# Kernel tuning notes

Hardware: AMD Instinct MI355X
Metric: run time of the kernel (lower is better)

Reference implementation:

```python
import jax, jax.numpy as jnp
import numpy as np

B, M, H = 8, 2048, 1024


def setup_inputs() -> dict:
    key = jax.random.key(0)
    k0, k1, k2, k3, k4 = jax.random.split(key, 5)
    return {
        "query": jax.random.normal(k0, (B, M, H), dtype=jnp.float32),
        "key": jax.random.normal(k1, (B, M, H), dtype=jnp.float32),
        "span": jax.random.uniform(k2, (B, M, 2), dtype=jnp.float32),
        "value": jax.random.normal(k3, (B, M, H), dtype=jnp.float32),
        "key_pe": jax.random.normal(k4, (1, H, M), dtype=jnp.float32),
    }


def reference(query, key, span, value, key_pe):
    # Faithful to the source's returned value:
    #   attn_cont (span-gathered version) is overwritten by the dense q @ k^T,
    #   and the scaled/softmaxed `attn` (content + positional) is computed but
    #   NEVER used for the output. The module returns attn_cont @ value with
    #   no scaling and no softmax. span / key_pe do not affect the output.
    attn_cont = jnp.einsum('bmh,bnh->bmn', query, key)  # [B, M, M]
    out = jnp.matmul(attn_cont, value)                   # [B, M, H]
    return out
```

## Files before the change

### kernel.cpp

```cpp
#include <hip/hip_runtime.h>
#include <hip/hip_bf16.h>

typedef __attribute__((ext_vector_type(4))) float f32x4;
typedef __attribute__((ext_vector_type(8))) short bf16x8;
typedef unsigned short u16;


__device__ __forceinline__ u16 f2bf(float f) {
  union { float f; unsigned int u; } v;
  v.f = f;
  unsigned int r = (v.u + 0x7fffu + ((v.u >> 16) & 1u)) >> 16;
  return (u16)r;
}

__device__ __forceinline__ void async16(const void* g, const void* l) {
  __builtin_amdgcn_global_load_lds(
      (const __attribute__((address_space(1))) unsigned int*)(unsigned long)g,
      (__attribute__((address_space(3))) unsigned int*)(unsigned int)(unsigned long)l,
      16, 0, 0);
}


__global__ __launch_bounds__(256) void cvt_plain(const float* __restrict__ in,
                                                 u16* __restrict__ out, int n4) {
  int stride = gridDim.x * blockDim.x;
  for (int i = blockIdx.x * blockDim.x + threadIdx.x; i < n4; i += stride) {
    f32x4 v = *(const f32x4*)(in + (long)i * 4);
    ushort4 o;
    o.x = f2bf(v.x); o.y = f2bf(v.y); o.z = f2bf(v.z); o.w = f2bf(v.w);
    *(ushort4*)(out + (long)i * 4) = o;
  }
}


__global__ __launch_bounds__(256) void cvt_transpose(const float* __restrict__ in,
                                                     u16* __restrict__ out,
                                                     int R, int C) {
  __shared__ u16 tile[64][68];
  const long bo = (long)blockIdx.z * (long)R * (long)C;
  const int r0 = blockIdx.y * 64;
  const int c0 = blockIdx.x * 64;
  const int t = threadIdx.x;
  const int tr = t >> 4;
  const int tc4 = (t & 15) * 4;

#pragma unroll
  for (int i = 0; i < 4; ++i) {
    int r = i * 16 + tr;
    f32x4 v = *(const f32x4*)(in + bo + (long)(r0 + r) * C + c0 + tc4);
    tile[tc4 + 0][r] = f2bf(v.x);
    tile[tc4 + 1][r] = f2bf(v.y);
    tile[tc4 + 2][r] = f2bf(v.z);
    tile[tc4 + 3][r] = f2bf(v.w);
  }
  __syncthreads();
#pragma unroll
  for (int i = 0; i < 4; ++i) {
    int c = i * 16 + tr;
    ushort4 u = *(const ushort4*)(&tile[c][tc4]);
    *(ushort4*)(out + bo + (long)(c0 + c) * R + r0 + tc4) = u;
  }
}


#define BM 128
#define BN 128
#define BK 32

template <bool BF16OUT>
__global__ __launch_bounds__(256, 4) void gemm_nt(const u16* __restrict__ A,
                                                  const u16* __restrict__ Bt,
                                                  void* __restrict__ Cv,
                                                  int M, int N, int K,
                                                  long sA, long sB, long sC,
                                                  int nTN) {
  __shared__ u16 As[2][BM][BK];
  __shared__ u16 Bs[2][BN][BK];

  const int bid  = blockIdx.x;
  const int b    = bid & 7;
  const int tile = bid >> 3;
  const int bn0 = (tile % nTN) * BN;
  const int bm0 = (tile / nTN) * BM;

  A  += (long)b * sA;
  Bt += (long)b * sB;

  const int tid  = threadIdx.x;
  const int lane = tid & 63;
  const int wave = tid >> 6;
  const int wr = wave >> 1;
  const int wc = wave & 1;
  const int l16 = lane & 15;
  const int kh  = lane >> 4;

  const u16* Abase = A + (long)bm0 * K;
  const u16* Bbase = Bt + (long)bn0 * K;

  const int u0 = wave * 64 + lane;

  f32x4 acc[4][4] = {};

  const int NT = K / BK;
  int cur = 0;

#pragma unroll
  for (int i = 0; i < 2; ++i) {
    int u = i * 256 + u0;
    async16(Abase + (long)(u >> 2) * K + (u & 3) * 8,
            (const char*)(&As[0][0][0]) + i * 4096 + wave * 1024);
    async16(Bbase + (long)(u >> 2) * K + (u & 3) * 8,
            (const char*)(&Bs[0][0][0]) + i * 4096 + wave * 1024);
  }
  asm volatile("s_waitcnt vmcnt(0)" ::: "memory");
  __syncthreads();

  for (int t = 0; t < NT; ++t) {
    if (t + 1 < NT) {
      const int k0 = (t + 1) * BK;
      const int nb = cur ^ 1;
#pragma unroll
      for (int i = 0; i < 2; ++i) {
        int u = i * 256 + u0;
        async16(Abase + k0 + (long)(u >> 2) * K + (u & 3) * 8,
                (const char*)(&As[nb][0][0]) + i * 4096 + wave * 1024);
        async16(Bbase + k0 + (long)(u >> 2) * K + (u & 3) * 8,
                (const char*)(&Bs[nb][0][0]) + i * 4096 + wave * 1024);
      }
    }

    bf16x8 af[4], bfr[4];
#pragma unroll
    for (int i = 0; i < 4; ++i) {
      af[i]  = *(const bf16x8*)(&As[cur][wr * 64 + i * 16 + l16][kh * 8]);
      bfr[i] = *(const bf16x8*)(&Bs[cur][wc * 64 + i * 16 + l16][kh * 8]);
    }
#pragma unroll
    for (int i = 0; i < 4; ++i)
#pragma unroll
      for (int j = 0; j < 4; ++j)
        acc[i][j] =
            __builtin_amdgcn_mfma_f32_16x16x32_bf16(af[i], bfr[j], acc[i][j], 0, 0, 0);

    asm volatile("s_waitcnt vmcnt(0)" ::: "memory");
    __syncthreads();
    cur ^= 1;
  }

  u16*   Cb = (u16*)Cv + (long)b * sC;
  float* Cf = (float*)Cv + (long)b * sC;
#pragma unroll
  for (int i = 0; i < 4; ++i) {
    const int gm = bm0 + wr * 64 + i * 16 + kh * 4;
#pragma unroll
    for (int j = 0; j < 4; ++j) {
      const int gn = bn0 + wc * 64 + j * 16 + l16;
#pragma unroll
      for (int r = 0; r < 4; ++r) {
        if (BF16OUT)
          Cb[(long)(gm + r) * N + gn] = f2bf(acc[i][j][r]);
        else
          Cf[(long)(gm + r) * N + gn] = acc[i][j][r];
      }
    }
  }
}


extern "C" void kernel_launch(void* const* d_in, const int* in_sizes, int n_in,
                              void* d_out, int out_size, void* d_ws, size_t ws_size,
                              hipStream_t stream) {
  const float* Q  = (const float*)d_in[0];
  const float* Kf = (const float*)d_in[1];
  const float* V  = (const float*)d_in[3];
  float* out = (float*)d_out;

  const int B = 8, M = 2048, H = 1024;
  const size_t bmh2 = (size_t)B * M * H * 2;

  char* ws = (char*)d_ws;
  u16* Qb = (u16*)(ws);
  u16* Kt = (u16*)(ws + bmh2);
  u16* Vt = (u16*)(ws + 2 * bmh2);
  u16* Pt = (u16*)(ws + 3 * bmh2);

  cvt_plain<<<2048, 256, 0, stream>>>(Q, Qb, B * M * H / 4);
  cvt_transpose<<<dim3(H / 64, M / 64, B), 256, 0, stream>>>(Kf, Kt, M, H);
  cvt_transpose<<<dim3(H / 64, M / 64, B), 256, 0, stream>>>(V, Vt, M, H);

  gemm_nt<true><<<B * (H / BM) * (H / BN), 256, 0, stream>>>(
      Vt, Kt, (void*)Pt, H, H, M, (long)H * M, (long)H * M, (long)H * H, H / BN);

  gemm_nt<false><<<B * (M / BM) * (H / BN), 256, 0, stream>>>(
      Qb, Pt, (void*)out, M, H, H, (long)M * H, (long)H * H, (long)M * H, H / BN);
}
```

Baseline: 151.7 us.

## Rewrite GEMM with 256x128 tiles, 8 waves, triple-buffered swizzled LDS pipeline

Replaces the 128x128x32 double-buffered GEMM with a 512-thread kernel using 256x128 tiles, BK=64, three LDS stages, and an XOR swizzle on LDS rows to avoid bank conflicts. Global-to-LDS async loads are interleaved between MFMA groups, with barriers and setprio so memory traffic overlaps compute. The aim is better data reuse per block, fewer bank conflicts and hidden load latency. In exchange it uses more LDS and registers per block and launches fewer blocks, which lowers occupancy.

```diff
diff --git a/kernel.cpp b/kernel.cpp
--- a/kernel.cpp
+++ b/kernel.cpp
@@ -63,104 +63,161 @@
 }
 
 
-#define BM 128
-#define BN 128
-#define BK 32
+#define ASTRIDE (256 * 64)
+#define BSTRIDE (128 * 64)
+
+#define LD_A(c, f, ks) (*(const bf16x8*)((const u16*)As + (c)*ASTRIDE + offA[f][ks]))
+#define LD_B(c, f, ks) (*(const bf16x8*)((const u16*)Bs + (c)*BSTRIDE + offB[f][ks]))
+#define STG_A(i, buf) async16(srcA[i], (const char*)As + (buf)*(ASTRIDE * 2) + dstA[i])
+#define STG_B(i, buf) async16(srcB[i], (const char*)Bs + (buf)*(BSTRIDE * 2) + dstB[i])
+#define MF(am, bn, fm, fn) \
+  acc[fm][fn] = __builtin_amdgcn_mfma_f32_16x16x32_bf16(am, bn, acc[fm][fn], 0, 0, 0)
 
 template <bool BF16OUT>
-__global__ __launch_bounds__(256, 4) void gemm_nt(const u16* __restrict__ A,
-                                                  const u16* __restrict__ Bt,
-                                                  void* __restrict__ Cv,
-                                                  int M, int N, int K,
-                                                  long sA, long sB, long sC,
-                                                  int nTN) {
-  __shared__ u16 As[2][BM][BK];
-  __shared__ u16 Bs[2][BN][BK];
+__global__ __launch_bounds__(512, 2) void gemm8(const u16* __restrict__ A,
+                                                const u16* __restrict__ Bt,
+                                                void* __restrict__ Cv,
+                                                int M, int N, int K,
+                                                long sA, long sB, long sC,
+                                                int nTN) {
+  __shared__ u16 As[3][256][64];
+  __shared__ u16 Bs[3][128][64];
 
   const int bid  = blockIdx.x;
   const int b    = bid & 7;
   const int tile = bid >> 3;
-  const int bn0 = (tile % nTN) * BN;
-  const int bm0 = (tile / nTN) * BM;
-
-  A  += (long)b * sA;
-  Bt += (long)b * sB;
+  const int bn0 = (tile % nTN) * 128;
+  const int bm0 = (tile / nTN) * 256;
+
+  const u16* Ab = A + (long)b * sA + (long)bm0 * K;
+  const u16* Bb = Bt + (long)b * sB + (long)bn0 * K;
 
   const int tid  = threadIdx.x;
   const int lane = tid & 63;
   const int wave = tid >> 6;
-  const int wr = wave >> 1;
-  const int wc = wave & 1;
-  const int l16 = lane & 15;
-  const int kh  = lane >> 4;
-
-  const u16* Abase = A + (long)bm0 * K;
-  const u16* Bbase = Bt + (long)bn0 * K;
-
-  const int u0 = wave * 64 + lane;
+  const int wr   = wave >> 1;
+  const int wc   = wave & 1;
+  const int l16  = lane & 15;
+  const int kh   = lane >> 4;
+
+  const char* srcA[4];
+  const char* srcB[2];
+  int dstA[4], dstB[2];
+#pragma unroll
+  for (int i = 0; i < 4; ++i) {
+    int u = tid + i * 512;
+    int row = u >> 3, sl = (u & 7) ^ (row & 7);
+    srcA[i] = (const char*)(Ab + (long)row * K) + sl * 16;
+    dstA[i] = u * 16;
+  }
+#pragma unroll
+  for (int i = 0; i < 2; ++i) {
+    int u = tid + i * 512;
+    int row = u >> 3, sl = (u & 7) ^ (row & 7);
+    srcB[i] = (const char*)(Bb + (long)row * K) + sl * 16;
+    dstB[i] = u * 16;
+  }
+
+  int offA[4][2], offB[4][2];
+#pragma unroll
+  for (int f = 0; f < 4; ++f) {
+    int rA = wr * 64 + f * 16 + l16;
+    int rB = wc * 64 + f * 16 + l16;
+#pragma unroll
+    for (int ks = 0; ks < 2; ++ks) {
+      offA[f][ks] = rA * 64 + (((ks * 4 + kh) ^ (rA & 7)) * 8);
+      offB[f][ks] = rB * 64 + (((ks * 4 + kh) ^ (rB & 7)) * 8);
+    }
+  }
 
   f32x4 acc[4][4] = {};
-
-  const int NT = K / BK;
-  int cur = 0;
-
-#pragma unroll
-  for (int i = 0; i < 2; ++i) {
-    int u = i * 256 + u0;
-    async16(Abase + (long)(u >> 2) * K + (u & 3) * 8,
-            (const char*)(&As[0][0][0]) + i * 4096 + wave * 1024);
-    async16(Bbase + (long)(u >> 2) * K + (u & 3) * 8,
-            (const char*)(&Bs[0][0][0]) + i * 4096 + wave * 1024);
-  }
-  asm volatile("s_waitcnt vmcnt(0)" ::: "memory");
-  __syncthreads();
-
+  const int NT = K / 64;
+
+#pragma unroll
+  for (int i = 0; i < 4; ++i) STG_A(i, 0);
+#pragma unroll
+  for (int i = 0; i < 2; ++i) STG_B(i, 0);
+#pragma unroll
+  for (int i = 0; i < 4; ++i) srcA[i] += 128;
+#pragma unroll
+  for (int i = 0; i < 2; ++i) srcB[i] += 128;
+#pragma unroll
+  for (int i = 0; i < 4; ++i) STG_A(i, 1);
+#pragma unroll
+  for (int i = 0; i < 2; ++i) STG_B(i, 1);
+#pragma unroll
+  for (int i = 0; i < 4; ++i) srcA[i] += 128;
+#pragma unroll
+  for (int i = 0; i < 2; ++i) srcB[i] += 128;
+  asm volatile("s_waitcnt vmcnt(6)" ::: "memory");
+  __builtin_amdgcn_s_barrier();
+
+  int c = 0, nb = 2;
   for (int t = 0; t < NT; ++t) {
-    if (t + 1 < NT) {
-      const int k0 = (t + 1) * BK;
-      const int nb = cur ^ 1;
-#pragma unroll
-      for (int i = 0; i < 2; ++i) {
-        int u = i * 256 + u0;
-        async16(Abase + k0 + (long)(u >> 2) * K + (u & 3) * 8,
-                (const char*)(&As[nb][0][0]) + i * 4096 + wave * 1024);
-        async16(Bbase + k0 + (long)(u >> 2) * K + (u & 3) * 8,
-                (const char*)(&Bs[nb][0][0]) + i * 4096 + wave * 1024);
-      }
-    }
-
-    bf16x8 af[4], bfr[4];
-#pragma unroll
-    for (int i = 0; i < 4; ++i) {
-      af[i]  = *(const bf16x8*)(&As[cur][wr * 64 + i * 16 + l16][kh * 8]);
-      bfr[i] = *(const bf16x8*)(&Bs[cur][wc * 64 + i * 16 + l16][kh * 8]);
-    }
-#pragma unroll
-    for (int i = 0; i < 4; ++i)
-#pragma unroll
-      for (int j = 0; j < 4; ++j)
-        acc[i][j] =
-            __builtin_amdgcn_mfma_f32_16x16x32_bf16(af[i], bfr[j], acc[i][j], 0, 0, 0);
-
-    asm volatile("s_waitcnt vmcnt(0)" ::: "memory");
-    __syncthreads();
-    cur ^= 1;
+    const bool st = (t + 2) < NT;
+
+    bf16x8 a0 = LD_A(c, 0, 0), a1 = LD_A(c, 1, 0);
+    bf16x8 b0 = LD_B(c, 0, 0), b1 = LD_B(c, 1, 0);
+    bf16x8 b2 = LD_B(c, 2, 0), b3 = LD_B(c, 3, 0);
+    if (st) { STG_A(0, nb); STG_A(1, nb); }
+    asm volatile("" ::: "memory");
+    __builtin_amdgcn_s_barrier();
+    __builtin_amdgcn_s_setprio(1);
+    MF(a0, b0, 0, 0); MF(a0, b1, 0, 1); MF(a0, b2, 0, 2); MF(a0, b3, 0, 3);
+    MF(a1, b0, 1, 0); MF(a1, b1, 1, 1); MF(a1, b2, 1, 2); MF(a1, b3, 1, 3);
+    __builtin_amdgcn_s_setprio(0);
+
+    bf16x8 a2 = LD_A(c, 2, 0), a3 = LD_A(c, 3, 0);
+    if (st) { STG_A(2, nb); STG_A(3, nb); }
+    asm volatile("" ::: "memory");
+    __builtin_amdgcn_s_barrier();
+    __builtin_amdgcn_s_setprio(1);
+    MF(a2, b0, 2, 0); MF(a2, b1, 2, 1); MF(a2, b2, 2, 2); MF(a2, b3, 2, 3);
+    MF(a3, b0, 3, 0); MF(a3, b1, 3, 1); MF(a3, b2, 3, 2); MF(a3, b3, 3, 3);
+    __builtin_amdgcn_s_setprio(0);
+
+    a0 = LD_A(c, 0, 1); a1 = LD_A(c, 1, 1);
+    b0 = LD_B(c, 0, 1); b1 = LD_B(c, 1, 1);
+    b2 = LD_B(c, 2, 1); b3 = LD_B(c, 3, 1);
+    if (st) STG_B(0, nb);
+    asm volatile("" ::: "memory");
+    __builtin_amdgcn_s_barrier();
+    __builtin_amdgcn_s_setprio(1);
+    MF(a0, b0, 0, 0); MF(a0, b1, 0, 1); MF(a0, b2, 0, 2); MF(a0, b3, 0, 3);
+    MF(a1, b0, 1, 0); MF(a1, b1, 1, 1); MF(a1, b2, 1, 2); MF(a1, b3, 1, 3);
+    __builtin_amdgcn_s_setprio(0);
+
+    a2 = LD_A(c, 2, 1); a3 = LD_A(c, 3, 1);
+    if (st) STG_B(1, nb);
+#pragma unroll
+    for (int i = 0; i < 4; ++i) srcA[i] += 128;
+#pragma unroll
+    for (int i = 0; i < 2; ++i) srcB[i] += 128;
+    if (st) asm volatile("s_waitcnt vmcnt(6)" ::: "memory");
+    else    asm volatile("s_waitcnt vmcnt(0)" ::: "memory");
+    asm volatile("s_waitcnt lgkmcnt(0)" ::: "memory");
+    __builtin_amdgcn_s_barrier();
+    __builtin_amdgcn_s_setprio(1);
+    MF(a2, b0, 2, 0); MF(a2, b1, 2, 1); MF(a2, b2, 2, 2); MF(a2, b3, 2, 3);
+    MF(a3, b0, 3, 0); MF(a3, b1, 3, 1); MF(a3, b2, 3, 2); MF(a3, b3, 3, 3);
+    __builtin_amdgcn_s_setprio(0);
+
+    c = (c == 2) ? 0 : c + 1;
+    nb = (nb == 2) ? 0 : nb + 1;
   }
 
   u16*   Cb = (u16*)Cv + (long)b * sC;
   float* Cf = (float*)Cv + (long)b * sC;
 #pragma unroll
-  for (int i = 0; i < 4; ++i) {
-    const int gm = bm0 + wr * 64 + i * 16 + kh * 4;
-#pragma unroll
-    for (int j = 0; j < 4; ++j) {
-      const int gn = bn0 + wc * 64 + j * 16 + l16;
+  for (int fm = 0; fm < 4; ++fm) {
+    const int gm = bm0 + wr * 64 + fm * 16 + kh * 4;
+#pragma unroll
+    for (int fn = 0; fn < 4; ++fn) {
+      const int gn = bn0 + wc * 64 + fn * 16 + l16;
 #pragma unroll
       for (int r = 0; r < 4; ++r) {
-        if (BF16OUT)
-          Cb[(long)(gm + r) * N + gn] = f2bf(acc[i][j][r]);
-        else
-          Cf[(long)(gm + r) * N + gn] = acc[i][j][r];
+        if (BF16OUT) Cb[(long)(gm + r) * N + gn] = f2bf(acc[fm][fn][r]);
+        else         Cf[(long)(gm + r) * N + gn] = acc[fm][fn][r];
       }
     }
   }
@@ -188,9 +245,11 @@
   cvt_transpose<<<dim3(H / 64, M / 64, B), 256, 0, stream>>>(Kf, Kt, M, H);
   cvt_transpose<<<dim3(H / 64, M / 64, B), 256, 0, stream>>>(V, Vt, M, H);
 
-  gemm_nt<true><<<B * (H / BM) * (H / BN), 256, 0, stream>>>(
-      Vt, Kt, (void*)Pt, H, H, M, (long)H * M, (long)H * M, (long)H * H, H / BN);
-
-  gemm_nt<false><<<B * (M / BM) * (H / BN), 256, 0, stream>>>(
-      Qb, Pt, (void*)out, M, H, H, (long)M * H, (long)H * H, (long)M * H, H / BN);
-}
+  gemm8<true><<<8 * (1024 / 256) * (1024 / 128), 512, 0, stream>>>(
+      Vt, Kt, (void*)Pt, 1024, 1024, 2048, (long)H * M, (long)H * M, (long)H * H,
+      1024 / 128);
+
+  gemm8<false><<<8 * (2048 / 256) * (1024 / 128), 512, 0, stream>>>(
+      Qb, Pt, (void*)out, 2048, 1024, 1024, (long)M * H, (long)H * H, (long)M * H,
+      1024 / 128);
+}
```

Result: faster. 143.3 us (-5.6%).

## Replace GEMM with 8-wave ping-pong pipelined kernel using larger swizzled tiles

Applied to the files above, without the earlier changes.

Replaces the 4-wave 128x128x32 double-buffered GEMM with an 8-wave kernel that uses larger tiles (128x256 and 256x256) and BK=64. The tiles are split into half-quadrants with XOR-swizzled LDS layout. Global-to-LDS loads are interleaved with MFMA quadrants, using fine-grained barriers, partial vmcnt waits and s_setprio, so memory traffic overlaps compute. This aims to cut LDS bank conflicts and global traffic per FLOP and to hide load latency, at the cost of higher register pressure and more barriers.

```diff
diff --git a/kernel.cpp b/kernel.cpp
--- a/kernel.cpp
+++ b/kernel.cpp
@@ -63,104 +63,175 @@
 }
 
 
-#define BM 128
-#define BN 128
-#define BK 32
-
-template <bool BF16OUT>
-__global__ __launch_bounds__(256, 4) void gemm_nt(const u16* __restrict__ A,
-                                                  const u16* __restrict__ Bt,
-                                                  void* __restrict__ Cv,
-                                                  int M, int N, int K,
-                                                  long sA, long sB, long sC,
-                                                  int nTN) {
-  __shared__ u16 As[2][BM][BK];
-  __shared__ u16 Bs[2][BN][BK];
-
-  const int bid  = blockIdx.x;
-  const int b    = bid & 7;
+#define BARRIER()                                   \
+  {                                                 \
+    asm volatile("" ::: "memory");                  \
+    __builtin_amdgcn_s_barrier();                   \
+    asm volatile("" ::: "memory");                  \
+  }
+
+#define STG_A(h, buf)                                                         \
+  {                                                                           \
+    _Pragma("unroll") for (int i_ = 0; i_ < LA; ++i_) {                       \
+      async16(Ab + aoff[h][i_],                                               \
+              (char*)&As[buf][h][0][0] + (tid + i_ * 512) * 16);              \
+      aoff[h][i_] += 128;                                                     \
+    }                                                                         \
+  }
+
+#define STG_B(h, buf)                                                         \
+  {                                                                           \
+    _Pragma("unroll") for (int i_ = 0; i_ < LB; ++i_) {                       \
+      async16(Bb + boff[h][i_],                                               \
+              (char*)&Bs[buf][h][0][0] + (tid + i_ * 512) * 16);              \
+      boff[h][i_] += 128;                                                     \
+    }                                                                         \
+  }
+
+#define LDA_Q(buf, qm)                                                        \
+  {                                                                           \
+    _Pragma("unroll") for (int f_ = 0; f_ < HM; ++f_) {                       \
+      areg[f_][0] = *(const bf16x8*)&As[buf][qm][wrA + f_ * 16][sw0];         \
+      areg[f_][1] = *(const bf16x8*)&As[buf][qm][wrA + f_ * 16][sw1];         \
+    }                                                                         \
+  }
+
+#define LDB_Q(buf, qn)                                                        \
+  {                                                                           \
+    _Pragma("unroll") for (int g_ = 0; g_ < HN; ++g_) {                       \
+      breg[qn * HN + g_][0] = *(const bf16x8*)&Bs[buf][qn][wcB + g_ * 16][sw0]; \
+      breg[qn * HN + g_][1] = *(const bf16x8*)&Bs[buf][qn][wcB + g_ * 16][sw1]; \
+    }                                                                         \
+  }
+
+#define MMA_Q(qm, qn)                                                         \
+  {                                                                           \
+    __builtin_amdgcn_s_setprio(1);                                            \
+    _Pragma("unroll") for (int f_ = 0; f_ < HM; ++f_)                         \
+    _Pragma("unroll") for (int g_ = 0; g_ < HN; ++g_)                         \
+    _Pragma("unroll") for (int k_ = 0; k_ < 2; ++k_)                          \
+      acc[qm * HM + f_][qn * HN + g_] =                                       \
+          __builtin_amdgcn_mfma_f32_16x16x32_bf16(                            \
+              areg[f_][k_], breg[qn * HN + g_][k_],                           \
+              acc[qm * HM + f_][qn * HN + g_], 0, 0, 0);                      \
+    __builtin_amdgcn_s_setprio(0);                                            \
+  }
+
+#define VMC_LA()                                                              \
+  {                                                                           \
+    if constexpr (LA == 2) asm volatile("s_waitcnt vmcnt(2)" ::: "memory");   \
+    else asm volatile("s_waitcnt vmcnt(1)" ::: "memory");                     \
+  }
+
+#define VMC_STEADY()                                                          \
+  {                                                                           \
+    if (more) VMC_LA()                                                        \
+    else asm volatile("s_waitcnt vmcnt(0)" ::: "memory");                     \
+  }
+
+#define TILE(cur, nxt, g01, g23, vm)                                          \
+  {                                                                           \
+                                          \
+    LDA_Q(cur, 0); LDB_Q(cur, 0);                                             \
+    if (g01) STG_A(1, nxt);                                                   \
+    BARRIER(); MMA_Q(0, 0); BARRIER();                                        \
+                                          \
+    LDB_Q(cur, 1);                                                            \
+    if (g01) STG_B(0, nxt);                                                   \
+    BARRIER(); MMA_Q(0, 1); BARRIER();                                        \
+                                          \
+    LDA_Q(cur, 1);                                                            \
+    if (g01) STG_B(1, nxt);                                                   \
+    BARRIER(); MMA_Q(1, 0); BARRIER();                                        \
+                          \
+    if (g23) STG_A(0, cur);                                                   \
+    vm;                                                                       \
+    BARRIER(); MMA_Q(1, 1); BARRIER();                                        \
+  }
+
+template <int BM, int BN, bool BF16OUT>
+__global__ __launch_bounds__(512, 2) void gemm8p(const u16* __restrict__ A,
+                                                 const u16* __restrict__ Bt,
+                                                 void* __restrict__ Cv,
+                                                 int N, int K,
+                                                 long sA, long sB, long sC,
+                                                 int nTN) {
+  constexpr int FM = BM / 32;
+  constexpr int FN = BN / 64;
+  constexpr int HM = FM / 2, HN = FN / 2;
+  constexpr int LA = BM / 128, LB = BN / 128;
+
+  __shared__ u16 As[2][2][BM / 2][64];
+  __shared__ u16 Bs[2][2][BN / 2][64];
+
+  const int bid = blockIdx.x;
+  const int b = bid & 7;
   const int tile = bid >> 3;
   const int bn0 = (tile % nTN) * BN;
   const int bm0 = (tile / nTN) * BM;
 
-  A  += (long)b * sA;
-  Bt += (long)b * sB;
-
-  const int tid  = threadIdx.x;
+  const char* Ab = (const char*)(A + (long)b * sA);
+  const char* Bb = (const char*)(Bt + (long)b * sB);
+
+  const int tid = threadIdx.x;
   const int lane = tid & 63;
   const int wave = tid >> 6;
-  const int wr = wave >> 1;
-  const int wc = wave & 1;
+  const int wr = wave >> 2;
+  const int wc = wave & 3;
   const int l16 = lane & 15;
-  const int kh  = lane >> 4;
-
-  const u16* Abase = A + (long)bm0 * K;
-  const u16* Bbase = Bt + (long)bn0 * K;
-
-  const int u0 = wave * 64 + lane;
-
-  f32x4 acc[4][4] = {};
-
-  const int NT = K / BK;
-  int cur = 0;
-
-#pragma unroll
-  for (int i = 0; i < 2; ++i) {
-    int u = i * 256 + u0;
-    async16(Abase + (long)(u >> 2) * K + (u & 3) * 8,
-            (const char*)(&As[0][0][0]) + i * 4096 + wave * 1024);
-    async16(Bbase + (long)(u >> 2) * K + (u & 3) * 8,
-            (const char*)(&Bs[0][0][0]) + i * 4096 + wave * 1024);
-  }
-  asm volatile("s_waitcnt vmcnt(0)" ::: "memory");
-  __syncthreads();
-
-  for (int t = 0; t < NT; ++t) {
-    if (t + 1 < NT) {
-      const int k0 = (t + 1) * BK;
-      const int nb = cur ^ 1;
-#pragma unroll
-      for (int i = 0; i < 2; ++i) {
-        int u = i * 256 + u0;
-        async16(Abase + k0 + (long)(u >> 2) * K + (u & 3) * 8,
-                (const char*)(&As[nb][0][0]) + i * 4096 + wave * 1024);
-        async16(Bbase + k0 + (long)(u >> 2) * K + (u & 3) * 8,
-                (const char*)(&Bs[nb][0][0]) + i * 4096 + wave * 1024);
-      }
+  const int kh = lane >> 4;
+
+  const int wrA = wr * (HM * 16) + l16;
+  const int wcB = wc * (HN * 16) + l16;
+  const int sw0 = (kh ^ (l16 & 7)) * 8;
+  const int sw1 = ((4 + kh) ^ (l16 & 7)) * 8;
+
+  int aoff[2][LA], boff[2][LB];
+#pragma unroll
+  for (int h = 0; h < 2; ++h)
+#pragma unroll
+    for (int i = 0; i < LA; ++i) {
+      int u = tid + i * 512;
+      int row = u >> 3, sl = (u & 7) ^ (row & 7);
+      aoff[h][i] = (bm0 + h * (BM / 2) + row) * (K * 2) + sl * 16;
     }
-
-    bf16x8 af[4], bfr[4];
-#pragma unroll
-    for (int i = 0; i < 4; ++i) {
-      af[i]  = *(const bf16x8*)(&As[cur][wr * 64 + i * 16 + l16][kh * 8]);
-      bfr[i] = *(const bf16x8*)(&Bs[cur][wc * 64 + i * 16 + l16][kh * 8]);
+#pragma unroll
+  for (int h = 0; h < 2; ++h)
+#pragma unroll
+    for (int i = 0; i < LB; ++i) {
+      int u = tid + i * 512;
+      int row = u >> 3, sl = (u & 7) ^ (row & 7);
+      boff[h][i] = (bn0 + h * (BN / 2) + row) * (K * 2) + sl * 16;
     }
-#pragma unroll
-    for (int i = 0; i < 4; ++i)
-#pragma unroll
-      for (int j = 0; j < 4; ++j)
-        acc[i][j] =
-            __builtin_amdgcn_mfma_f32_16x16x32_bf16(af[i], bfr[j], acc[i][j], 0, 0, 0);
-
-    asm volatile("s_waitcnt vmcnt(0)" ::: "memory");
-    __syncthreads();
-    cur ^= 1;
+
+  f32x4 acc[FM][FN] = {};
+  bf16x8 areg[HM][2], breg[FN][2];
+
+  const int NT = K / 64;
+
+  STG_A(0, 0); STG_A(1, 0); STG_B(0, 0); STG_B(1, 0);
+  STG_A(0, 1);
+  VMC_LA();
+  BARRIER();
+
+  for (int it = 0; it < NT / 2; ++it) {
+    const bool more = (it + 1 < NT / 2);
+    TILE(0, 1, true, more, VMC_STEADY());
+    TILE(1, 0, more, more, VMC_STEADY());
   }
 
   u16*   Cb = (u16*)Cv + (long)b * sC;
   float* Cf = (float*)Cv + (long)b * sC;
 #pragma unroll
-  for (int i = 0; i < 4; ++i) {
-    const int gm = bm0 + wr * 64 + i * 16 + kh * 4;
-#pragma unroll
-    for (int j = 0; j < 4; ++j) {
-      const int gn = bn0 + wc * 64 + j * 16 + l16;
+  for (int fm = 0; fm < FM; ++fm) {
+    const int gm = bm0 + (fm / HM) * (BM / 2) + wr * (HM * 16) + (fm % HM) * 16 + kh * 4;
+#pragma unroll
+    for (int fn = 0; fn < FN; ++fn) {
+      const int gn = bn0 + (fn / HN) * (BN / 2) + wc * (HN * 16) + (fn % HN) * 16 + l16;
 #pragma unroll
       for (int r = 0; r < 4; ++r) {
-        if (BF16OUT)
-          Cb[(long)(gm + r) * N + gn] = f2bf(acc[i][j][r]);
-        else
-          Cf[(long)(gm + r) * N + gn] = acc[i][j][r];
+        if (BF16OUT) Cb[(long)(gm + r) * N + gn] = f2bf(acc[fm][fn][r]);
+        else         Cf[(long)(gm + r) * N + gn] = acc[fm][fn][r];
       }
     }
   }
@@ -188,9 +259,9 @@
   cvt_transpose<<<dim3(H / 64, M / 64, B), 256, 0, stream>>>(Kf, Kt, M, H);
   cvt_transpose<<<dim3(H / 64, M / 64, B), 256, 0, stream>>>(V, Vt, M, H);
 
-  gemm_nt<true><<<B * (H / BM) * (H / BN), 256, 0, stream>>>(
-      Vt, Kt, (void*)Pt, H, H, M, (long)H * M, (long)H * M, (long)H * H, H / BN);
-
-  gemm_nt<false><<<B * (M / BM) * (H / BN), 256, 0, stream>>>(
-      Qb, Pt, (void*)out, M, H, H, (long)M * H, (long)H * H, (long)M * H, H / BN);
-}
+  gemm8p<128, 256, true><<<256, 512, 0, stream>>>(
+      Vt, Kt, (void*)Pt, 1024, 2048, (long)H * M, (long)H * M, (long)H * H, 4);
+
+  gemm8p<256, 256, false><<<256, 512, 0, stream>>>(
+      Qb, Pt, (void*)out, 1024, 1024, (long)M * H, (long)H * H, (long)M * H, 4);
+}
```

Result: faster. 141.0 us (-7.1%).
